# Kernel optimization log

Measured on AMD Instinct MI355X. Metric: run time of the kernel, lower is better.

The kernel has to match this reference:

```python
import jax, jax.numpy as jnp
import numpy as np

D_MODEL = 512
NUM_HEADS = 8
HEAD_DIM = D_MODEL // NUM_HEADS


def setup_inputs() -> dict:
    key = jax.random.key(0)
    ks = jax.random.split(key, 12)
    B, S = 4, 2048
    s = 1.0 / np.sqrt(D_MODEL)  # torch Linear default init scale (uniform bound)
    def lin(k1, k2):
        W = jax.random.uniform(k1, (D_MODEL, D_MODEL), jnp.float32, -s, s)
        b = jax.random.uniform(k2, (D_MODEL,), jnp.float32, -s, s)
        return W, b
    Wq, bq = lin(ks[0], ks[1])
    Wk, bk = lin(ks[2], ks[3])
    Wv, bv = lin(ks[4], ks[5])
    Wo, bo = lin(ks[6], ks[7])
    return {
        "q": jax.random.normal(ks[8], (B, S, D_MODEL), jnp.float32),
        "k": jax.random.normal(ks[9], (B, S, D_MODEL), jnp.float32),
        "v": jax.random.normal(ks[10], (B, S, D_MODEL), jnp.float32),
        "mask": jnp.ones((B, 1, 1, S), jnp.int32),
        "Wq": Wq, "bq": bq, "Wk": Wk, "bk": bk,
        "Wv": Wv, "bv": bv, "Wo": Wo, "bo": bo,
    }


def reference(q, k, v, mask, Wq, bq, Wk, bk, Wv, bv, Wo, bo):
    B, S, _ = q.shape
    scale = np.sqrt(HEAD_DIM).astype(np.float32)
    # projections; torch Linear: x @ W.T + b
    def split_heads(x):  # [B,S,D] -> [B,H,S,hd]
        return x.reshape(B, S, NUM_HEADS, HEAD_DIM).transpose(0, 2, 1, 3)
    Q = split_heads(q @ Wq.T + bq)
    K = split_heads(k @ Wk.T + bk)
    V = split_heads(v @ Wv.T + bv)
    scores = jnp.einsum('bhqd,bhkd->bhqk', Q, K) / scale
    # NOTE: source calls scores.masked_fill(...) non-in-place and discards the
    # result, so the mask has no effect on the math.
    attn = jax.nn.softmax(scores, axis=-1)
    # dropout is identity in eval / deterministic baseline
    out = jnp.einsum('bhqk,bhkd->bhqd', attn, V)
    out = out.transpose(0, 2, 1, 3).reshape(B, S, D_MODEL)
    return out @ Wo.T + bo
```

## Files before the change

kernel.cpp:

```cpp
#include <hip/hip_runtime.h>

#define NB 4
#define NH 8
#define NS 2048
#define ND 512
#define HD 64
#define KVB 64

typedef __attribute__((ext_vector_type(8))) short s16x8;
typedef __attribute__((ext_vector_type(4))) float f32x4;
typedef __attribute__((ext_vector_type(16))) float f32x16;
typedef __attribute__((ext_vector_type(4))) unsigned int u32x4;

#define L2E 1.44269504088896f
#define CSC (0.125f * L2E)

__device__ __forceinline__ unsigned short f2bf(float f) {
  unsigned int u = __builtin_bit_cast(unsigned int, f);
  u += 0x7FFFu + ((u >> 16) & 1u);
  return (unsigned short)(u >> 16);
}
__device__ __forceinline__ unsigned cvtpk_bf16(float lo, float hi) {
  unsigned r;
  asm("v_cvt_pk_bf16_f32 %0, %1, %2" : "=v"(r) : "v"(lo), "v"(hi));
  return r;
}
__device__ __forceinline__ void pl32swap(unsigned& a, unsigned& b) {
  asm("v_permlane32_swap_b32 %0, %1" : "+v"(a), "+v"(b));
}
__device__ __forceinline__ float exp2s(float x) {
  float r;
  asm("v_exp_f32 %0, %1" : "=v"(r) : "v"(x));
  return r;
}
__device__ __forceinline__ void gl_lds16(const void* g, void* l) {
  __builtin_amdgcn_global_load_lds(
      (const __attribute__((address_space(1))) unsigned int*)g,
      (__attribute__((address_space(3))) unsigned int*)l, 16, 0, 0);
}

__global__ __launch_bounds__(256) void convw_kernel(
    const float* __restrict__ Wq, const float* __restrict__ Wk,
    const float* __restrict__ Wv, const float* __restrict__ Wo,
    unsigned short* __restrict__ Wc)
{
  const int bid = blockIdx.x;
  const int m = bid >> 7;
  const float* __restrict__ src = (m == 0) ? Wq : (m == 1) ? Wk : (m == 2) ? Wv : Wo;
  const float sc = (m == 0) ? CSC : 1.0f;
  const int base = (bid & 127) * 2048 + threadIdx.x * 8;
  float4 a = *(const float4*)(src + base);
  float4 b = *(const float4*)(src + base + 4);
  u32x4 o;
  o[0] = cvtpk_bf16(a.x * sc, a.y * sc);
  o[1] = cvtpk_bf16(a.z * sc, a.w * sc);
  o[2] = cvtpk_bf16(b.x * sc, b.y * sc);
  o[3] = cvtpk_bf16(b.z * sc, b.w * sc);
  *(u32x4*)(Wc + (size_t)m * 262144 + base) = o;
}

__global__ __launch_bounds__(256, 2) void proj_kernel(
    const float* __restrict__ qin, const float* __restrict__ kin,
    const float* __restrict__ vin,
    const float* __restrict__ bq, const float* __restrict__ bk,
    const float* __restrict__ bv,
    const unsigned short* __restrict__ Wc,
    unsigned short* __restrict__ Qp, unsigned short* __restrict__ Kp,
    unsigned short* __restrict__ VpT)
{
  __shared__ short sm[32768];
  short* As0 = sm;
  short* Bs0 = sm + 16384;

  const int z = blockIdx.z;
  const float* __restrict__ X    = (z == 0) ? qin : (z == 1) ? kin : vin;
  const float* __restrict__ bias = (z == 0) ? bq  : (z == 1) ? bk  : bv;
  const unsigned short* __restrict__ W = Wc + (size_t)z * 262144;

  const int n0 = blockIdx.x * 128;
  const int m0 = blockIdx.y * 128;
  const int t = threadIdx.x;
  const int lane = t & 63, w = t >> 6;
  const int wrow = (w >> 1) * 64, wcol = (w & 1) * 64;
  const int l15 = lane & 15, l4 = lane >> 4;

  const int arow = t >> 3;
  const int ac = t & 7;
  const int grow = lane >> 3;
  const int gc = (lane & 7) ^ grow;

  f32x4 acc[4][4];
  const f32x4 z4 = {0.f, 0.f, 0.f, 0.f};
#pragma unroll
  for (int m = 0; m < 4; ++m)
#pragma unroll
    for (int n = 0; n < 4; ++n) acc[m][n] = z4;

  float4 ra[4][2];
#define LOADA(kt)                                                              \
  {                                                                            \
    _Pragma("unroll") for (int j = 0; j < 4; ++j) {                            \
      const float* p = X + (size_t)(m0 + arow + j * 32) * ND + (kt) * 64 + ac * 8; \
      ra[j][0] = *(const float4*)p;                                            \
      ra[j][1] = *(const float4*)(p + 4);                                      \
    }                                                                          \
  }
#define AWRITE(bufv)                                                           \
  {                                                                            \
    char* dst = (char*)(As0 + (bufv) * 8192);                                  \
    _Pragma("unroll") for (int j = 0; j < 4; ++j) {                            \
      const int row = arow + j * 32;                                           \
      u32x4 pk;                                                                \
      pk[0] = cvtpk_bf16(ra[j][0].x, ra[j][0].y);                              \
      pk[1] = cvtpk_bf16(ra[j][0].z, ra[j][0].w);                              \
      pk[2] = cvtpk_bf16(ra[j][1].x, ra[j][1].y);                              \
      pk[3] = cvtpk_bf16(ra[j][1].z, ra[j][1].w);                              \
      *(u32x4*)(dst + row * 128 + ((ac << 4) ^ ((row & 7) << 4))) = pk;        \
    }                                                                          \
  }
#define BDMA(kt, bufv)                                                         \
  {                                                                            \
    short* dst = Bs0 + (bufv) * 8192 + w * 2048;                               \
    _Pragma("unroll") for (int j = 0; j < 4; ++j) {                            \
      const unsigned short* src =                                              \
          W + (size_t)(n0 + w * 32 + j * 8 + grow) * ND + (kt) * 64 + gc * 8;  \
      gl_lds16(src, dst + j * 512);                                            \
    }                                                                          \
  }

  LOADA(0)
  AWRITE(0)
  BDMA(0, 0)
  int buf = 0;
  for (int kt = 0; kt < 8; ++kt) {
    __syncthreads();
    if (kt < 7) {
      BDMA(kt + 1, buf ^ 1)
      LOADA(kt + 1)
    }
    const char* Ab = (const char*)(As0 + buf * 8192);
    const char* Bb = (const char*)(Bs0 + buf * 8192);
    __builtin_amdgcn_s_setprio(1);
#pragma unroll
    for (int kk = 0; kk < 2; ++kk) {
      s16x8 af[4], bfr[4];
#pragma unroll
      for (int m = 0; m < 4; ++m) {
        const int r = wrow + m * 16 + l15;
        af[m] = *(const s16x8*)(Ab + r * 128 + (((kk * 4 + l4) << 4) ^ ((r & 7) << 4)));
      }
#pragma unroll
      for (int n = 0; n < 4; ++n) {
        const int r = wcol + n * 16 + l15;
        bfr[n] = *(const s16x8*)(Bb + r * 128 + (((kk * 4 + l4) << 4) ^ ((r & 7) << 4)));
      }
#pragma unroll
      for (int m = 0; m < 4; ++m)
#pragma unroll
        for (int n = 0; n < 4; ++n)
          acc[m][n] = __builtin_amdgcn_mfma_f32_16x16x32_bf16(af[m], bfr[n], acc[m][n], 0, 0, 0);
    }
    __builtin_amdgcn_s_setprio(0);
    if (kt < 7) AWRITE(buf ^ 1)
    buf ^= 1;
  }
#undef LOADA
#undef AWRITE
#undef BDMA

  __syncthreads();
  short* T = sm;
  const int b = m0 >> 11, sb = m0 & 2047;

  if (z != 2) {
    const float bsc = (z == 0) ? CSC : 1.0f;
#pragma unroll
    for (int n = 0; n < 4; ++n) {
      const int cp = wcol + n * 16 + l15;
      const float bb = bias[n0 + cp] * bsc;
#pragma unroll
      for (int m = 0; m < 4; ++m)
#pragma unroll
        for (int r = 0; r < 4; ++r) {
          const int sp = wrow + m * 16 + l4 * 4 + r;
          T[sp * 136 + cp] = (short)f2bf(acc[m][n][r] + bb);
        }
    }
    __syncthreads();
    unsigned short* P = (z == 0) ? Qp : Kp;
#pragma unroll
    for (int i = 0; i < 8; ++i) {
      const int ch = i * 256 + t;
      const int row = ch >> 4, c = ch & 15;
      const int h = (n0 >> 6) + (c >> 3), dd = (c & 7) * 8;
      s16x8 vv = *(const s16x8*)(T + row * 136 + c * 8);
      *(s16x8*)(P + ((size_t)(b * NH + h) * NS + sb + row) * HD + dd) = vv;
    }
  } else {
#pragma unroll
    for (int n = 0; n < 4; ++n) {
      const int cp = wcol + n * 16 + l15;
      const float bb = bias[n0 + cp];
#pragma unroll
      for (int m = 0; m < 4; ++m) {
        const int sp = wrow + m * 16 + l4 * 4;
        *(unsigned*)(T + cp * 136 + sp)     = cvtpk_bf16(acc[m][n][0] + bb, acc[m][n][1] + bb);
        *(unsigned*)(T + cp * 136 + sp + 2) = cvtpk_bf16(acc[m][n][2] + bb, acc[m][n][3] + bb);
      }
    }
    __syncthreads();
#pragma unroll
    for (int i = 0; i < 8; ++i) {
      const int ch = i * 256 + t;
      const int row = ch >> 4, c = ch & 15;
      s16x8 vv = *(const s16x8*)(T + row * 136 + c * 8);
      *(s16x8*)(VpT + ((size_t)(b * 512 + n0 + row)) * NS + sb + c * 8) = vv;
    }
  }
}

__global__ __launch_bounds__(256, 2) void attn_kernel(
    unsigned short* Qp, const unsigned short* __restrict__ Kp,
    const unsigned short* __restrict__ VpT)
{
  __shared__ short sm[32768];
  short* Ks = sm;
  short* Vs = sm + 16384;

  const int bh = blockIdx.y;
  const int q0 = blockIdx.x * 128;
  const int t = threadIdx.x;
  const int lane = t & 63, w = t >> 6;
  const int l31 = lane & 31, hi = lane >> 5;
  const int swz = (l31 & 7) << 4;

  const unsigned short* Qbase = Qp + ((size_t)bh * NS + q0 + w * 32) * HD;
  const unsigned short* Kbase = Kp + (size_t)bh * NS * HD;
  const unsigned short* Vbase = VpT + (size_t)bh * HD * NS;

  s16x8 qf[4];
#pragma unroll
  for (int kf = 0; kf < 4; ++kf)
    qf[kf] = *(const s16x8*)(Qbase + l31 * HD + kf * 16 + hi * 8);

  const int srow = lane >> 3;
  const int scol = (lane & 7) ^ srow;
  const unsigned short* ksrc0 = Kbase + (size_t)(w * 16 + srow) * HD + scol * 8;
  const unsigned short* vsrc0 = Vbase + (size_t)(w * 16 + srow) * NS + scol * 8;

  float lrun = 0.f;
  f32x16 acc[2];
#pragma unroll
  for (int n = 0; n < 2; ++n)
#pragma unroll
    for (int r = 0; r < 16; ++r) acc[n][r] = 0.f;

#define STAGE(p, bufv)                                                         \
  {                                                                            \
    _Pragma("unroll") for (int u = 0; u < 2; ++u) {                            \
      const int tt = 2 * (p) + u;                                              \
      const unsigned short* kp_ = ksrc0 + (size_t)tt * KVB * HD;               \
      const unsigned short* vp_ = vsrc0 + tt * KVB;                            \
      short* kd = Ks + (bufv) * 8192 + u * 4096 + w * 1024;                    \
      short* vd = Vs + (bufv) * 8192 + u * 4096 + w * 1024;                    \
      gl_lds16(kp_, kd);                                                       \
      gl_lds16(kp_ + 8 * HD, kd + 512);                                        \
      gl_lds16(vp_, vd);                                                       \
      gl_lds16(vp_ + 8 * NS, vd + 512);                                        \
    }                                                                          \
  }

  STAGE(0, 0)
  int buf = 0;
  for (int p = 0; p < 16; ++p) {
    __syncthreads();
    if (p < 15) STAGE(p + 1, buf ^ 1)

    const char* Kb = (const char*)(Ks + buf * 8192);
    const char* Vb = (const char*)(Vs + buf * 8192);

    f32x16 sA[2], sB[2];
#pragma unroll
    for (int t2 = 0; t2 < 2; ++t2)
#pragma unroll
      for (int r = 0; r < 16; ++r) { sA[t2][r] = 0.f; sB[t2][r] = 0.f; }

    __builtin_amdgcn_s_setprio(1);
#pragma unroll
    for (int t2 = 0; t2 < 2; ++t2)
#pragma unroll
      for (int kf = 0; kf < 4; ++kf) {
        s16x8 ka = *(const s16x8*)(Kb + (t2 * 32 + l31) * 128 +
                                   (((kf * 2 + hi) << 4) ^ swz));
        sA[t2] = __builtin_amdgcn_mfma_f32_32x32x16_bf16(ka, qf[kf], sA[t2], 0, 0, 0);
      }
#pragma unroll
    for (int t2 = 0; t2 < 2; ++t2)
#pragma unroll
      for (int kf = 0; kf < 4; ++kf) {
        s16x8 kb = *(const s16x8*)(Kb + 8192 + (t2 * 32 + l31) * 128 +
                                   (((kf * 2 + hi) << 4) ^ swz));
        sB[t2] = __builtin_amdgcn_mfma_f32_32x32x16_bf16(kb, qf[kf], sB[t2], 0, 0, 0);
      }
    __builtin_amdgcn_s_setprio(0);

    float pvA[32], pvB[32];
#pragma unroll
    for (int t2 = 0; t2 < 2; ++t2)
#pragma unroll
      for (int r = 0; r < 16; ++r) pvA[t2 * 16 + r] = exp2s(sA[t2][r]);

    s16x8 pafA[4];
#pragma unroll
    for (int idx = 0; idx < 4; ++idx) {
      const float* pp = &pvA[idx * 8];
      unsigned x0 = cvtpk_bf16(pp[0], pp[1]);
      unsigned y0 = cvtpk_bf16(pp[4], pp[5]);
      unsigned x1 = cvtpk_bf16(pp[2], pp[3]);
      unsigned y1 = cvtpk_bf16(pp[6], pp[7]);
      pl32swap(x0, y0);
      pl32swap(x1, y1);
      u32x4 fw = {x0, x1, y0, y1};
      pafA[idx] = __builtin_bit_cast(s16x8, fw);
    }
    __builtin_amdgcn_s_setprio(1);
#pragma unroll
    for (int n = 0; n < 2; ++n)
#pragma unroll
      for (int idx = 0; idx < 4; ++idx) {
        s16x8 va = *(const s16x8*)(Vb + (n * 32 + l31) * 128 +
                                   (((idx * 2 + hi) << 4) ^ swz));
        acc[n] = __builtin_amdgcn_mfma_f32_32x32x16_bf16(va, pafA[idx], acc[n], 0, 0, 0);
      }
    __builtin_amdgcn_s_setprio(0);

#pragma unroll
    for (int t2 = 0; t2 < 2; ++t2)
#pragma unroll
      for (int r = 0; r < 16; ++r) pvB[t2 * 16 + r] = exp2s(sB[t2][r]);

    s16x8 pafB[4];
#pragma unroll
    for (int idx = 0; idx < 4; ++idx) {
      const float* pp = &pvB[idx * 8];
      unsigned x0 = cvtpk_bf16(pp[0], pp[1]);
      unsigned y0 = cvtpk_bf16(pp[4], pp[5]);
      unsigned x1 = cvtpk_bf16(pp[2], pp[3]);
      unsigned y1 = cvtpk_bf16(pp[6], pp[7]);
      pl32swap(x0, y0);
      pl32swap(x1, y1);
      u32x4 fw = {x0, x1, y0, y1};
      pafB[idx] = __builtin_bit_cast(s16x8, fw);
    }
    __builtin_amdgcn_s_setprio(1);
#pragma unroll
    for (int n = 0; n < 2; ++n)
#pragma unroll
      for (int idx = 0; idx < 4; ++idx) {
        s16x8 va = *(const s16x8*)(Vb + 8192 + (n * 32 + l31) * 128 +
                                   (((idx * 2 + hi) << 4) ^ swz));
        acc[n] = __builtin_amdgcn_mfma_f32_32x32x16_bf16(va, pafB[idx], acc[n], 0, 0, 0);
      }
    __builtin_amdgcn_s_setprio(0);

    float s32[32];
#pragma unroll
    for (int i = 0; i < 32; ++i) s32[i] = pvA[i] + pvB[i];
    float s16_[16];
#pragma unroll
    for (int i = 0; i < 16; ++i) s16_[i] = s32[i] + s32[i + 16];
    float s8[8];
#pragma unroll
    for (int i = 0; i < 8; ++i) s8[i] = s16_[i] + s16_[i + 8];
    float s4[4];
#pragma unroll
    for (int i = 0; i < 4; ++i) s4[i] = s8[i] + s8[i + 4];
    float psum = (s4[0] + s4[1]) + (s4[2] + s4[3]);
    lrun += psum + __shfl_xor(psum, 32);

    buf ^= 1;
  }
#undef STAGE

  __syncthreads();
  short* Od = sm;
  const float rinv = 1.0f / lrun;
  const int rw = w * 32 + l31;
#pragma unroll
  for (int n = 0; n < 2; ++n)
#pragma unroll
    for (int g = 0; g < 4; ++g) {
      unsigned lo  = cvtpk_bf16(acc[n][g * 4 + 0] * rinv, acc[n][g * 4 + 1] * rinv);
      unsigned hi2 = cvtpk_bf16(acc[n][g * 4 + 2] * rinv, acc[n][g * 4 + 3] * rinv);
      const int dby = (n * 64 + g * 16 + hi * 8) ^ swz;
      *(unsigned*)((char*)Od + rw * 128 + dby)     = lo;
      *(unsigned*)((char*)Od + rw * 128 + (dby ^ 4)) = hi2;
    }
  __syncthreads();

#pragma unroll
  for (int j = 0; j < 4; ++j) {
    const int ch = j * 256 + t;
    const int q = ch >> 3, c = ch & 7;
    s16x8 vdat = *(const s16x8*)((const char*)Od + q * 128 + ((c ^ (q & 7)) << 4));
    *(s16x8*)(Qp + ((size_t)bh * NS + q0 + q) * HD + c * 8) = vdat;
  }
}

__global__ __launch_bounds__(256) void oproj_kernel(
    const unsigned short* __restrict__ Op, const unsigned short* __restrict__ Wc,
    const float* __restrict__ bo, float* __restrict__ out)
{
  __shared__ short sm[32768];
  short* A0 = sm;
  short* B0 = sm + 16384;

  const int n0 = blockIdx.x * 128;
  const int m0 = blockIdx.y * 128;
  const int b = m0 >> 11, sb = m0 & 2047;
  const int t = threadIdx.x;
  const int lane = t & 63, w = t >> 6;
  const int wrow = (w >> 1) * 64, wcol = (w & 1) * 64;
  const int l15 = lane & 15, l4 = lane >> 4;
  const int grow = lane >> 3, gc = (lane & 7) ^ grow;
  const unsigned short* Wo16 = Wc + 3 * 262144;

  f32x4 acc[4][4];
  const f32x4 z4 = {0.f, 0.f, 0.f, 0.f};
#pragma unroll
  for (int m = 0; m < 4; ++m)
#pragma unroll
    for (int n = 0; n < 4; ++n) acc[m][n] = z4;

#define ODMA(kt, bufv)                                                         \
  {                                                                            \
    short* ad = A0 + (bufv) * 8192 + w * 2048;                                 \
    short* bd = B0 + (bufv) * 8192 + w * 2048;                                 \
    _Pragma("unroll") for (int j = 0; j < 4; ++j) {                            \
      const unsigned short* as =                                               \
          Op + ((size_t)(b * NH + (kt)) * NS + sb + w * 32 + j * 8 + grow) * HD + gc * 8; \
      gl_lds16(as, ad + j * 512);                                              \
      const unsigned short* bs =                                               \
          Wo16 + (size_t)(n0 + w * 32 + j * 8 + grow) * ND + (kt) * 64 + gc * 8; \
      gl_lds16(bs, bd + j * 512);                                              \
    }                                                                          \
  }

  ODMA(0, 0)
  int buf = 0;
  for (int kt = 0; kt < 8; ++kt) {
    __syncthreads();
    if (kt < 7) ODMA(kt + 1, buf ^ 1)
    const char* Ab = (const char*)(A0 + buf * 8192);
    const char* Bb = (const char*)(B0 + buf * 8192);
    __builtin_amdgcn_s_setprio(1);
#pragma unroll
    for (int kk = 0; kk < 2; ++kk) {
      s16x8 af[4], bfr[4];
#pragma unroll
      for (int m = 0; m < 4; ++m) {
        const int r = wrow + m * 16 + l15;
        af[m] = *(const s16x8*)(Ab + r * 128 + (((kk * 4 + l4) << 4) ^ ((r & 7) << 4)));
      }
#pragma unroll
      for (int n = 0; n < 4; ++n) {
        const int r = wcol + n * 16 + l15;
        bfr[n] = *(const s16x8*)(Bb + r * 128 + (((kk * 4 + l4) << 4) ^ ((r & 7) << 4)));
      }
#pragma unroll
      for (int m = 0; m < 4; ++m)
#pragma unroll
        for (int n = 0; n < 4; ++n)
          acc[m][n] = __builtin_amdgcn_mfma_f32_16x16x32_bf16(af[m], bfr[n], acc[m][n], 0, 0, 0);
    }
    __builtin_amdgcn_s_setprio(0);
    buf ^= 1;
  }
#undef ODMA

#pragma unroll
  for (int n = 0; n < 4; ++n) {
    const int col = n0 + wcol + n * 16 + l15;
    const float bb = bo[col];
#pragma unroll
    for (int m = 0; m < 4; ++m)
#pragma unroll
      for (int r = 0; r < 4; ++r) {
        const int mg = m0 + wrow + m * 16 + l4 * 4 + r;
        out[(size_t)mg * ND + col] = acc[m][n][r] + bb;
      }
  }
}

extern "C" void kernel_launch(void* const* d_in, const int* in_sizes, int n_in,
                              void* d_out, int out_size, void* d_ws, size_t ws_size,
                              hipStream_t stream) {
  const float* q  = (const float*)d_in[0];
  const float* k  = (const float*)d_in[1];
  const float* v  = (const float*)d_in[2];
  const float* Wq = (const float*)d_in[4];
  const float* bq = (const float*)d_in[5];
  const float* Wk = (const float*)d_in[6];
  const float* bk = (const float*)d_in[7];
  const float* Wv = (const float*)d_in[8];
  const float* bv = (const float*)d_in[9];
  const float* Wo = (const float*)d_in[10];
  const float* bo = (const float*)d_in[11];
  float* out = (float*)d_out;

  const size_t headElems = (size_t)NB * NH * NS * HD;
  unsigned short* Qp  = (unsigned short*)d_ws;
  unsigned short* Kp  = Qp + headElems;
  unsigned short* VpT = Kp + headElems;
  unsigned short* Wc  = VpT + headElems;

  hipLaunchKernelGGL(convw_kernel, dim3(512), dim3(256), 0, stream,
                     Wq, Wk, Wv, Wo, Wc);
  hipLaunchKernelGGL(proj_kernel, dim3(4, 64, 3), dim3(256), 0, stream,
                     q, k, v, bq, bk, bv, Wc, Qp, Kp, VpT);
  hipLaunchKernelGGL(attn_kernel, dim3(16, 32), dim3(256), 0, stream,
                     Qp, Kp, VpT);
  hipLaunchKernelGGL(oproj_kernel, dim3(4, 64), dim3(256), 0, stream,
                     Qp, Wc, bo, out);
}
```

Baseline: 186.7 us.

## Pre-convert activations to bf16 and DMA both GEMM operands directly into LDS

Extends the weight conversion kernel to also convert the q/k/v activations to bf16 in a workspace buffer. The projection GEMM then loads both A and B tiles with global_load_lds DMA instead of loading fp32 A into registers, converting, and writing to LDS. This removes the register staging and conversion work from the GEMM main loop and halves the bytes read per A tile. The cost is an extra full pass that reads the fp32 activations and writes a bf16 copy.

After: 183.3 us. Within noise of the previous version (-1.8%).

```diff
diff --git a/kernel.cpp b/kernel.cpp
--- a/kernel.cpp
+++ b/kernel.cpp
@@ -39,16 +39,31 @@
       (__attribute__((address_space(3))) unsigned int*)l, 16, 0, 0);
 }
 
-__global__ __launch_bounds__(256) void convw_kernel(
+__global__ __launch_bounds__(256) void conv_kernel(
+    const float* __restrict__ xq, const float* __restrict__ xk,
+    const float* __restrict__ xv,
     const float* __restrict__ Wq, const float* __restrict__ Wk,
     const float* __restrict__ Wv, const float* __restrict__ Wo,
-    unsigned short* __restrict__ Wc)
+    unsigned short* __restrict__ Wc, unsigned short* __restrict__ Xc)
 {
   const int bid = blockIdx.x;
-  const int m = bid >> 7;
-  const float* __restrict__ src = (m == 0) ? Wq : (m == 1) ? Wk : (m == 2) ? Wv : Wo;
-  const float sc = (m == 0) ? CSC : 1.0f;
-  const int base = (bid & 127) * 2048 + threadIdx.x * 8;
+  const float* __restrict__ src;
+  unsigned short* __restrict__ dst;
+  float sc = 1.0f;
+  int base;
+  if (bid < 512) {
+    const int m = bid >> 7;
+    src = (m == 0) ? Wq : (m == 1) ? Wk : (m == 2) ? Wv : Wo;
+    if (m == 0) sc = CSC;
+    base = (bid & 127) * 2048 + threadIdx.x * 8;
+    dst = Wc + (size_t)m * 262144;
+  } else {
+    const int idx = bid - 512;
+    const int zi = idx >> 11;
+    src = (zi == 0) ? xq : (zi == 1) ? xk : xv;
+    base = (idx & 2047) * 2048 + threadIdx.x * 8;
+    dst = Xc + (size_t)zi * 4194304;
+  }
   float4 a = *(const float4*)(src + base);
   float4 b = *(const float4*)(src + base + 4);
   u32x4 o;
@@ -56,12 +71,11 @@
   o[1] = cvtpk_bf16(a.z * sc, a.w * sc);
   o[2] = cvtpk_bf16(b.x * sc, b.y * sc);
   o[3] = cvtpk_bf16(b.z * sc, b.w * sc);
-  *(u32x4*)(Wc + (size_t)m * 262144 + base) = o;
+  *(u32x4*)(dst + base) = o;
 }
 
 __global__ __launch_bounds__(256, 2) void proj_kernel(
-    const float* __restrict__ qin, const float* __restrict__ kin,
-    const float* __restrict__ vin,
+    const unsigned short* __restrict__ Xc,
     const float* __restrict__ bq, const float* __restrict__ bk,
     const float* __restrict__ bv,
     const unsigned short* __restrict__ Wc,
@@ -73,8 +87,8 @@
   short* Bs0 = sm + 16384;
 
   const int z = blockIdx.z;
-  const float* __restrict__ X    = (z == 0) ? qin : (z == 1) ? kin : vin;
-  const float* __restrict__ bias = (z == 0) ? bq  : (z == 1) ? bk  : bv;
+  const float* __restrict__ bias = (z == 0) ? bq : (z == 1) ? bk : bv;
+  const unsigned short* __restrict__ X = Xc + (size_t)z * 4194304;
   const unsigned short* __restrict__ W = Wc + (size_t)z * 262144;
 
   const int n0 = blockIdx.x * 128;
@@ -83,11 +97,7 @@
   const int lane = t & 63, w = t >> 6;
   const int wrow = (w >> 1) * 64, wcol = (w & 1) * 64;
   const int l15 = lane & 15, l4 = lane >> 4;
-
-  const int arow = t >> 3;
-  const int ac = t & 7;
-  const int grow = lane >> 3;
-  const int gc = (lane & 7) ^ grow;
+  const int grow = lane >> 3, gc = (lane & 7) ^ grow;
 
   f32x4 acc[4][4];
   const f32x4 z4 = {0.f, 0.f, 0.f, 0.f};
@@ -96,48 +106,25 @@
 #pragma unroll
     for (int n = 0; n < 4; ++n) acc[m][n] = z4;
 
-  float4 ra[4][2];
-#define LOADA(kt)                                                              \
+#define PDMA(kt, bufv)                                                         \
   {                                                                            \
+    short* ad = As0 + (bufv) * 8192 + w * 2048;                                \
+    short* bd = Bs0 + (bufv) * 8192 + w * 2048;                                \
     _Pragma("unroll") for (int j = 0; j < 4; ++j) {                            \
-      const float* p = X + (size_t)(m0 + arow + j * 32) * ND + (kt) * 64 + ac * 8; \
-      ra[j][0] = *(const float4*)p;                                            \
-      ra[j][1] = *(const float4*)(p + 4);                                      \
+      const unsigned short* as =                                               \
+          X + (size_t)(m0 + w * 32 + j * 8 + grow) * ND + (kt) * 64 + gc * 8;  \
+      gl_lds16(as, ad + j * 512);                                              \
+      const unsigned short* bs =                                               \
+          W + (size_t)(n0 + w * 32 + j * 8 + grow) * ND + (kt) * 64 + gc * 8;  \
+      gl_lds16(bs, bd + j * 512);                                              \
     }                                                                          \
   }
-#define AWRITE(bufv)                                                           \
-  {                                                                            \
-    char* dst = (char*)(As0 + (bufv) * 8192);                                  \
-    _Pragma("unroll") for (int j = 0; j < 4; ++j) {                            \
-      const int row = arow + j * 32;                                           \
-      u32x4 pk;                                                                \
-      pk[0] = cvtpk_bf16(ra[j][0].x, ra[j][0].y);                              \
-      pk[1] = cvtpk_bf16(ra[j][0].z, ra[j][0].w);                              \
-      pk[2] = cvtpk_bf16(ra[j][1].x, ra[j][1].y);                              \
-      pk[3] = cvtpk_bf16(ra[j][1].z, ra[j][1].w);                              \
-      *(u32x4*)(dst + row * 128 + ((ac << 4) ^ ((row & 7) << 4))) = pk;        \
-    }                                                                          \
-  }
-#define BDMA(kt, bufv)                                                         \
-  {                                                                            \
-    short* dst = Bs0 + (bufv) * 8192 + w * 2048;                               \
-    _Pragma("unroll") for (int j = 0; j < 4; ++j) {                            \
-      const unsigned short* src =                                              \
-          W + (size_t)(n0 + w * 32 + j * 8 + grow) * ND + (kt) * 64 + gc * 8;  \
-      gl_lds16(src, dst + j * 512);                                            \
-    }                                                                          \
-  }
-
-  LOADA(0)
-  AWRITE(0)
-  BDMA(0, 0)
+
+  PDMA(0, 0)
   int buf = 0;
   for (int kt = 0; kt < 8; ++kt) {
     __syncthreads();
-    if (kt < 7) {
-      BDMA(kt + 1, buf ^ 1)
-      LOADA(kt + 1)
-    }
+    if (kt < 7) PDMA(kt + 1, buf ^ 1)
     const char* Ab = (const char*)(As0 + buf * 8192);
     const char* Bb = (const char*)(Bs0 + buf * 8192);
     __builtin_amdgcn_s_setprio(1);
@@ -161,12 +148,9 @@
           acc[m][n] = __builtin_amdgcn_mfma_f32_16x16x32_bf16(af[m], bfr[n], acc[m][n], 0, 0, 0);
     }
     __builtin_amdgcn_s_setprio(0);
-    if (kt < 7) AWRITE(buf ^ 1)
     buf ^= 1;
   }
-#undef LOADA
-#undef AWRITE
-#undef BDMA
+#undef PDMA
 
   __syncthreads();
   short* T = sm;
@@ -393,7 +377,7 @@
       unsigned lo  = cvtpk_bf16(acc[n][g * 4 + 0] * rinv, acc[n][g * 4 + 1] * rinv);
       unsigned hi2 = cvtpk_bf16(acc[n][g * 4 + 2] * rinv, acc[n][g * 4 + 3] * rinv);
       const int dby = (n * 64 + g * 16 + hi * 8) ^ swz;
-      *(unsigned*)((char*)Od + rw * 128 + dby)     = lo;
+      *(unsigned*)((char*)Od + rw * 128 + dby)       = lo;
       *(unsigned*)((char*)Od + rw * 128 + (dby ^ 4)) = hi2;
     }
   __syncthreads();
@@ -513,11 +497,12 @@
   unsigned short* Kp  = Qp + headElems;
   unsigned short* VpT = Kp + headElems;
   unsigned short* Wc  = VpT + headElems;
-
-  hipLaunchKernelGGL(convw_kernel, dim3(512), dim3(256), 0, stream,
-                     Wq, Wk, Wv, Wo, Wc);
+  unsigned short* Xc  = Wc + 4 * 262144;
+
+  hipLaunchKernelGGL(conv_kernel, dim3(6656), dim3(256), 0, stream,
+                     q, k, v, Wq, Wk, Wv, Wo, Wc, Xc);
   hipLaunchKernelGGL(proj_kernel, dim3(4, 64, 3), dim3(256), 0, stream,
-                     q, k, v, bq, bk, bv, Wc, Qp, Kp, VpT);
+                     Xc, bq, bk, bv, Wc, Qp, Kp, VpT);
   hipLaunchKernelGGL(attn_kernel, dim3(16, 32), dim3(256), 0, stream,
                      Qp, Kp, VpT);
   hipLaunchKernelGGL(oproj_kernel, dim3(4, 64), dim3(256), 0, stream,
```

## Load fp32 A tiles via direct-to-LDS DMA and remap blocks for XCD locality

Applied to the files above, without the earlier changes.

The projection kernel now streams fp32 activation tiles straight into LDS with global-to-LDS loads, then converts them to bf16 fragments in registers, instead of staging them through registers and writing bf16 to LDS. This is meant to cut the VGPR pressure and the load-convert-store latency on the A path. All three kernels also remap block IDs so that blocks sharing data are grouped onto the same XCD, improving L2 reuse. The cost is a single-buffered fp32 A tile plus an extra barrier per k-step, which limits how much the loads can overlap with compute.

New measurement: 188.2 us. About the same (+0.8%).

```diff
diff --git a/kernel.cpp b/kernel.cpp
--- a/kernel.cpp
+++ b/kernel.cpp
@@ -69,25 +69,25 @@
     unsigned short* __restrict__ VpT)
 {
   __shared__ short sm[32768];
-  short* As0 = sm;
   short* Bs0 = sm + 16384;
 
-  const int z = blockIdx.z;
+  const int o = blockIdx.z * 256 + blockIdx.y * 4 + blockIdx.x;
+  const int wg = (o & 7) * 96 + (o >> 3);
+  const int z  = wg >> 8;
+  const int m_ = (wg & 255) >> 2;
+  const int n_ = wg & 3;
+
   const float* __restrict__ X    = (z == 0) ? qin : (z == 1) ? kin : vin;
   const float* __restrict__ bias = (z == 0) ? bq  : (z == 1) ? bk  : bv;
   const unsigned short* __restrict__ W = Wc + (size_t)z * 262144;
 
-  const int n0 = blockIdx.x * 128;
-  const int m0 = blockIdx.y * 128;
+  const int n0 = n_ * 128;
+  const int m0 = m_ * 128;
   const int t = threadIdx.x;
   const int lane = t & 63, w = t >> 6;
   const int wrow = (w >> 1) * 64, wcol = (w & 1) * 64;
   const int l15 = lane & 15, l4 = lane >> 4;
-
-  const int arow = t >> 3;
-  const int ac = t & 7;
-  const int grow = lane >> 3;
-  const int gc = (lane & 7) ^ grow;
+  const int grow = lane >> 3, gc = (lane & 7) ^ grow;
 
   f32x4 acc[4][4];
   const f32x4 z4 = {0.f, 0.f, 0.f, 0.f};
@@ -96,59 +96,59 @@
 #pragma unroll
     for (int n = 0; n < 4; ++n) acc[m][n] = z4;
 
-  float4 ra[4][2];
-#define LOADA(kt)                                                              \
+#define ADMA(kt)                                                               \
   {                                                                            \
-    _Pragma("unroll") for (int j = 0; j < 4; ++j) {                            \
-      const float* p = X + (size_t)(m0 + arow + j * 32) * ND + (kt) * 64 + ac * 8; \
-      ra[j][0] = *(const float4*)p;                                            \
-      ra[j][1] = *(const float4*)(p + 4);                                      \
-    }                                                                          \
-  }
-#define AWRITE(bufv)                                                           \
-  {                                                                            \
-    char* dst = (char*)(As0 + (bufv) * 8192);                                  \
-    _Pragma("unroll") for (int j = 0; j < 4; ++j) {                            \
-      const int row = arow + j * 32;                                           \
-      u32x4 pk;                                                                \
-      pk[0] = cvtpk_bf16(ra[j][0].x, ra[j][0].y);                              \
-      pk[1] = cvtpk_bf16(ra[j][0].z, ra[j][0].w);                              \
-      pk[2] = cvtpk_bf16(ra[j][1].x, ra[j][1].y);                              \
-      pk[3] = cvtpk_bf16(ra[j][1].z, ra[j][1].w);                              \
-      *(u32x4*)(dst + row * 128 + ((ac << 4) ^ ((row & 7) << 4))) = pk;        \
+    const float* xb = X + (size_t)(m0 + w * 32) * ND + (kt) * 64;              \
+    char* ad = (char*)sm + w * 8192;                                           \
+    _Pragma("unroll") for (int j = 0; j < 8; ++j) {                            \
+      const int i = j * 64 + lane;                                             \
+      const int rw_ = i >> 4, cc = i & 15;                                     \
+      gl_lds16(xb + (size_t)rw_ * ND + ((cc ^ (rw_ & 15)) << 2), ad + j * 1024); \
     }                                                                          \
   }
 #define BDMA(kt, bufv)                                                         \
   {                                                                            \
-    short* dst = Bs0 + (bufv) * 8192 + w * 2048;                               \
+    short* bd = Bs0 + (bufv) * 8192 + w * 2048;                                \
     _Pragma("unroll") for (int j = 0; j < 4; ++j) {                            \
-      const unsigned short* src =                                              \
+      const unsigned short* bs =                                               \
           W + (size_t)(n0 + w * 32 + j * 8 + grow) * ND + (kt) * 64 + gc * 8;  \
-      gl_lds16(src, dst + j * 512);                                            \
+      gl_lds16(bs, bd + j * 512);                                              \
     }                                                                          \
   }
 
-  LOADA(0)
-  AWRITE(0)
+  ADMA(0)
   BDMA(0, 0)
   int buf = 0;
   for (int kt = 0; kt < 8; ++kt) {
     __syncthreads();
+
+    s16x8 af2[2][4];
+#pragma unroll
+    for (int kk = 0; kk < 2; ++kk)
+#pragma unroll
+      for (int m = 0; m < 4; ++m) {
+        const int r = wrow + m * 16 + l15;
+        const int cb = kk * 8 + l4 * 2;
+        f32x4 lo = *(const f32x4*)((const char*)sm + r * 256 + ((cb ^ (r & 15)) << 4));
+        f32x4 hi = *(const f32x4*)((const char*)sm + r * 256 + (((cb + 1) ^ (r & 15)) << 4));
+        u32x4 pk;
+        pk[0] = cvtpk_bf16(lo[0], lo[1]);
+        pk[1] = cvtpk_bf16(lo[2], lo[3]);
+        pk[2] = cvtpk_bf16(hi[0], hi[1]);
+        pk[3] = cvtpk_bf16(hi[2], hi[3]);
+        af2[kk][m] = __builtin_bit_cast(s16x8, pk);
+      }
+    __syncthreads();
+
     if (kt < 7) {
+      ADMA(kt + 1)
       BDMA(kt + 1, buf ^ 1)
-      LOADA(kt + 1)
-    }
-    const char* Ab = (const char*)(As0 + buf * 8192);
+    }
     const char* Bb = (const char*)(Bs0 + buf * 8192);
     __builtin_amdgcn_s_setprio(1);
 #pragma unroll
     for (int kk = 0; kk < 2; ++kk) {
-      s16x8 af[4], bfr[4];
-#pragma unroll
-      for (int m = 0; m < 4; ++m) {
-        const int r = wrow + m * 16 + l15;
-        af[m] = *(const s16x8*)(Ab + r * 128 + (((kk * 4 + l4) << 4) ^ ((r & 7) << 4)));
-      }
+      s16x8 bfr[4];
 #pragma unroll
       for (int n = 0; n < 4; ++n) {
         const int r = wcol + n * 16 + l15;
@@ -158,14 +158,12 @@
       for (int m = 0; m < 4; ++m)
 #pragma unroll
         for (int n = 0; n < 4; ++n)
-          acc[m][n] = __builtin_amdgcn_mfma_f32_16x16x32_bf16(af[m], bfr[n], acc[m][n], 0, 0, 0);
+          acc[m][n] = __builtin_amdgcn_mfma_f32_16x16x32_bf16(af2[kk][m], bfr[n], acc[m][n], 0, 0, 0);
     }
     __builtin_amdgcn_s_setprio(0);
-    if (kt < 7) AWRITE(buf ^ 1)
     buf ^= 1;
   }
-#undef LOADA
-#undef AWRITE
+#undef ADMA
 #undef BDMA
 
   __syncthreads();
@@ -227,8 +225,11 @@
   short* Ks = sm;
   short* Vs = sm + 16384;
 
-  const int bh = blockIdx.y;
-  const int q0 = blockIdx.x * 128;
+  const int o = blockIdx.y * 16 + blockIdx.x;
+  const int wg = (o & 7) * 64 + (o >> 3);
+  const int bh = wg >> 4;
+  const int q0 = (wg & 15) * 128;
+
   const int t = threadIdx.x;
   const int lane = t & 63, w = t >> 6;
   const int l31 = lane & 31, hi = lane >> 5;
@@ -393,7 +394,7 @@
       unsigned lo  = cvtpk_bf16(acc[n][g * 4 + 0] * rinv, acc[n][g * 4 + 1] * rinv);
       unsigned hi2 = cvtpk_bf16(acc[n][g * 4 + 2] * rinv, acc[n][g * 4 + 3] * rinv);
       const int dby = (n * 64 + g * 16 + hi * 8) ^ swz;
-      *(unsigned*)((char*)Od + rw * 128 + dby)     = lo;
+      *(unsigned*)((char*)Od + rw * 128 + dby)       = lo;
       *(unsigned*)((char*)Od + rw * 128 + (dby ^ 4)) = hi2;
     }
   __syncthreads();
@@ -415,8 +416,10 @@
   short* A0 = sm;
   short* B0 = sm + 16384;
 
-  const int n0 = blockIdx.x * 128;
-  const int m0 = blockIdx.y * 128;
+  const int o = blockIdx.y * 4 + blockIdx.x;
+  const int wg = (o & 7) * 32 + (o >> 3);
+  const int n0 = (wg & 3) * 128;
+  const int m0 = (wg >> 2) * 128;
   const int b = m0 >> 11, sb = m0 & 2047;
   const int t = threadIdx.x;
   const int lane = t & 63, w = t >> 6;
```
